# Kernel tuning notes

Measured on AMD Instinct MI355X. Metric: run time of the kernel, lower is better.

The kernel has to match this reference:

```python
import jax, jax.numpy as jnp
import numpy as np

D_MODEL, N_GROUPS, N_EXPERTS = 512, 8, 8
TOP_K_L1, TOP_K_L2 = 2, 2
BATCH, SEQ = 2, 512


def setup_inputs() -> dict:
    key = jax.random.key(0)
    ks = jax.random.split(key, 6)
    d, G, E = D_MODEL, N_GROUPS, N_EXPERTS
    scale = 0.02
    x = jax.random.normal(ks[0], (BATCH, SEQ, d), dtype=jnp.float32)
    g1 = jax.random.normal(ks[1], (d, G), dtype=jnp.float32) * scale          # level-1 gate (no bias)
    g2 = jax.random.normal(ks[2], (G, d, E), dtype=jnp.float32) * scale       # per-group level-2 gate (no bias)
    W1 = jax.random.normal(ks[3], (G, E, d, 2 * d), dtype=jnp.float32) * scale
    b1 = jnp.zeros((G, E, 2 * d), dtype=jnp.float32)
    W2 = jax.random.normal(ks[4], (G, E, 2 * d, d), dtype=jnp.float32) * scale
    b2 = jnp.zeros((G, E, d), dtype=jnp.float32)
    return {"x": x, "g1": g1, "g2": g2, "W1": W1, "b1": b1, "W2": W2, "b2": b2}


def reference(x, g1, g2, W1, b1, W2, b2):
    B, S, d = x.shape
    G, E = g1.shape[1], g2.shape[2]
    xt = x.reshape(-1, d)  # [T, d]

    # ---- level-1 routing (groups) ----
    logits1 = xt @ g1                                   # [T, G]
    v1, i1 = jax.lax.top_k(logits1, TOP_K_L1)           # [T, k1]
    w1 = jax.nn.softmax(v1.astype(jnp.float32), axis=-1).astype(x.dtype)
    # dense combine weights: top-k indices are unique per token, so one-hot sum
    # is exactly the original gather/index_add_ math.
    c1 = jnp.sum(jax.nn.one_hot(i1, G, dtype=x.dtype) * w1[..., None], axis=1)  # [T, G]

    # ---- level-2 routing (experts within each group) ----
    logits2 = jnp.einsum('td,gde->tge', xt, g2)         # [T, G, E]
    v2, i2 = jax.lax.top_k(logits2, TOP_K_L2)           # [T, G, k2]
    w2 = jax.nn.softmax(v2.astype(jnp.float32), axis=-1).astype(x.dtype)
    c2 = jnp.sum(jax.nn.one_hot(i2, E, dtype=x.dtype) * w2[..., None], axis=2)  # [T, G, E]

    # ---- expert MLPs (Linear -> ReLU -> Linear), all experts, combined by weights ----
    h = jax.nn.relu(jnp.einsum('td,gedh->tgeh', xt, W1) + b1)   # [T, G, E, 2d]
    y = jnp.einsum('tgeh,gehd->tged', h, W2) + b2               # [T, G, E, d]

    group_out = jnp.einsum('tged,tge->tgd', y, c2)              # level-2 combine
    out = jnp.einsum('tgd,tg->td', group_out, c1)               # level-1 combine
    return out.reshape(B, S, d)
```

## Files before the change

### kernel.cpp

```cpp
#include <hip/hip_runtime.h>
#include <hip/hip_bf16.h>

#define D_M   512
#define H_M   1024
#define G_N   8
#define E_N   8
#define T_N   1024
#define NEXP  64
#define CAP   1024

#define LDK   520

typedef __attribute__((ext_vector_type(8))) short bf16x8;
typedef __attribute__((ext_vector_type(4))) float f32x4;
typedef __attribute__((ext_vector_type(4))) unsigned int u32x4;

__device__ __forceinline__ unsigned pack2(float a, float b) {
  unsigned r;
  asm("v_cvt_pk_bf16_f32 %0, %1, %2" : "=v"(r) : "v"(a), "v"(b));
  return r;
}
__device__ __forceinline__ unsigned short f2bf(float f) {
  unsigned u = __builtin_bit_cast(unsigned, f);
  u = (u + 0x7fffu + ((u >> 16) & 1u)) >> 16;
  return (unsigned short)u;
}

__global__ __launch_bounds__(64) void k_route(
    const float* __restrict__ x, const float* __restrict__ g1,
    const float* __restrict__ g2, float* __restrict__ slotW,
    int* __restrict__ counts, int* __restrict__ list) {
  __shared__ float xs[D_M];
  __shared__ float l2s[G_N][E_N];
  __shared__ float l1s[G_N];
  __shared__ float l1part[G_N][8];
  const int t = blockIdx.x;
  const int lane = threadIdx.x;
  const float* xr = x + (size_t)t * D_M;
  for (int i = lane; i < D_M; i += 64) xs[i] = xr[i];
  __syncthreads();
  {
    const int g = lane >> 3, e = lane & 7;
    const float* gp = g2 + (size_t)g * D_M * E_N + e;
    float acc = 0.f;
    #pragma unroll 8
    for (int i = 0; i < D_M; i++) acc += xs[i] * gp[(size_t)i * E_N];
    l2s[g][e] = acc;
  }
  {
    const int g = lane >> 3, c = lane & 7;
    float acc = 0.f;
    #pragma unroll 8
    for (int i = c * 64; i < c * 64 + 64; i++) acc += xs[i] * g1[(size_t)i * G_N + g];
    l1part[g][c] = acc;
  }
  __syncthreads();
  if (lane < G_N) {
    float s = 0.f;
    #pragma unroll
    for (int c = 0; c < 8; c++) s += l1part[lane][c];
    l1s[lane] = s;
  }
  __syncthreads();
  if (lane == 0) {
    int a1 = 0;
    for (int g = 1; g < G_N; g++) if (l1s[g] > l1s[a1]) a1 = g;
    int a2 = (a1 == 0) ? 1 : 0;
    for (int g = 0; g < G_N; g++) if (g != a1 && l1s[g] > l1s[a2]) a2 = g;
    const float m = l1s[a1];
    float w1a = __expf(l1s[a1] - m), w1b = __expf(l1s[a2] - m);
    const float inv = 1.f / (w1a + w1b);
    w1a *= inv; w1b *= inv;
    const int gsel[2] = {a1, a2};
    const float wsel[2] = {w1a, w1b};
    for (int a = 0; a < 2; a++) {
      const int g = gsel[a];
      int e1 = 0;
      for (int e = 1; e < E_N; e++) if (l2s[g][e] > l2s[g][e1]) e1 = e;
      int e2 = (e1 == 0) ? 1 : 0;
      for (int e = 0; e < E_N; e++) if (e != e1 && l2s[g][e] > l2s[g][e2]) e2 = e;
      const float mm = l2s[g][e1];
      float ua = __expf(l2s[g][e1] - mm), ub = __expf(l2s[g][e2] - mm);
      const float uin = 1.f / (ua + ub);
      ua *= uin; ub *= uin;
      const int ge0 = g * E_N + e1;
      const int ge1 = g * E_N + e2;
      slotW[t * 4 + a * 2 + 0] = wsel[a] * ua;
      slotW[t * 4 + a * 2 + 1] = wsel[a] * ub;
      int p0 = atomicAdd(&counts[ge0], 1);
      list[ge0 * CAP + p0] = t * 4 + a * 2 + 0;
      int p1 = atomicAdd(&counts[ge1], 1);
      list[ge1 * CAP + p1] = t * 4 + a * 2 + 1;
    }
  }
}

__global__ __launch_bounds__(256, 1) void k_mlp1(
    const float* __restrict__ x, const float* __restrict__ W1,
    const float* __restrict__ b1, const int* __restrict__ counts,
    const int* __restrict__ list, unsigned short* __restrict__ h_ws) {
  const int ge = blockIdx.x >> 4;
  const int jt = blockIdx.x & 15;
  const int jbase = jt * 64;
  const int n = counts[ge];
  if (n == 0) return;
  __shared__ unsigned short wl[4 * 16 * 64 * 8];
  __shared__ unsigned short xl[64 * LDK];
  __shared__ int tokTS[64];
  const int tid = threadIdx.x;
  const int lane = tid & 63, wave = tid >> 6;
  const int m16 = lane & 15, quad = lane >> 4;

  const float bv = b1[ge * H_M + jbase + wave * 16 + m16];

  {
    const float* Wg = W1 + (size_t)ge * (D_M * H_M) + jbase;
    const int rgrp = tid >> 4;
    const int lidx = tid & 15;
    const int wp = lidx >> 2;
    const int m16b = (lidx & 3) * 4;
    #pragma unroll 4
    for (int pass = 0; pass < 32; pass++) {
      const int r = pass * 16 + rgrp;
      f32x4 v = *(const f32x4*)(Wg + (size_t)r * H_M + lidx * 4);
      const int s = r >> 5, q = (r >> 3) & 3, i = r & 7;
      unsigned p0 = pack2(v.x, v.y), p1 = pack2(v.z, v.w);
      unsigned short* base = &wl[((wp * 16 + s) * 64 + q * 16 + m16b) * 8 + i];
      base[0 * 8] = (unsigned short)p0;
      base[1 * 8] = (unsigned short)(p0 >> 16);
      base[2 * 8] = (unsigned short)p1;
      base[3 * 8] = (unsigned short)(p1 >> 16);
    }
  }

  for (int t0 = 0; t0 < n; t0 += 64) {
    __syncthreads();
    if (tid < 64) {
      int idx = t0 + tid;
      tokTS[tid] = list[ge * CAP + (idx < n ? idx : n - 1)];
    }
    __syncthreads();
    {
      const int trow = tid >> 2;
      const int kb = (tid & 3) * 4;
      const float* xr = x + (size_t)(tokTS[trow] >> 2) * D_M + kb;
      unsigned short* dst = &xl[trow * LDK + kb];
      #pragma unroll 8
      for (int rep = 0; rep < 32; rep++) {
        f32x4 v = *(const f32x4*)(xr + rep * 16);
        uint2 p = { pack2(v.x, v.y), pack2(v.z, v.w) };
        *(uint2*)(dst + rep * 16) = p;
      }
    }
    __syncthreads();

    f32x4 acc[4] = {};
    #pragma unroll
    for (int s = 0; s < 16; s++) {
      bf16x8 wfrag = *(const bf16x8*)&wl[((wave * 16 + s) * 64 + lane) * 8];
      #pragma unroll
      for (int mt = 0; mt < 4; mt++) {
        bf16x8 af = *(bf16x8*)&xl[(mt * 16 + m16) * LDK + s * 32 + quad * 8];
        acc[mt] = __builtin_amdgcn_mfma_f32_16x16x32_bf16(af, wfrag, acc[mt], 0, 0, 0);
      }
    }
    #pragma unroll
    for (int mt = 0; mt < 4; mt++)
      #pragma unroll
      for (int i = 0; i < 4; i++) {
        const int tr = mt * 16 + quad * 4 + i;
        if (t0 + tr < n) {
          const int ts = tokTS[tr];
          float v = acc[mt][i] + bv;
          h_ws[(size_t)ts * H_M + jbase + wave * 16 + m16] = f2bf(v > 0.f ? v : 0.f);
        }
      }
  }
}

__global__ __launch_bounds__(256, 1) void k_mlp2(
    const unsigned short* __restrict__ h_ws, const float* __restrict__ W2,
    const float* __restrict__ b2, const int* __restrict__ counts,
    const int* __restrict__ list, float* __restrict__ y0,
    float* __restrict__ y1) {
  const int ge = blockIdx.x >> 4;
  const int jt = (blockIdx.x >> 1) & 7;
  const int jbase = jt * 64;
  const int ks = blockIdx.x & 1;
  const int n = counts[ge];
  if (n == 0) return;
  __shared__ unsigned short wl[4 * 16 * 64 * 8];
  __shared__ unsigned short xl[64 * LDK];
  __shared__ int tokTS[64];
  const int tid = threadIdx.x;
  const int lane = tid & 63, wave = tid >> 6;
  const int m16 = lane & 15, quad = lane >> 4;

  const float bv = ks == 0 ? b2[ge * D_M + jbase + wave * 16 + m16] : 0.f;
  float* yk = ks == 0 ? y0 : y1;

  {
    const float* Wg = W2 + (size_t)ge * (H_M * D_M) + (size_t)(ks * 512) * D_M + jbase;
    const int rgrp = tid >> 4;
    const int lidx = tid & 15;
    const int wp = lidx >> 2;
    const int m16b = (lidx & 3) * 4;
    #pragma unroll 4
    for (int pass = 0; pass < 32; pass++) {
      const int r = pass * 16 + rgrp;
      f32x4 v = *(const f32x4*)(Wg + (size_t)r * D_M + lidx * 4);
      const int s = r >> 5, q = (r >> 3) & 3, i = r & 7;
      unsigned p0 = pack2(v.x, v.y), p1 = pack2(v.z, v.w);
      unsigned short* base = &wl[((wp * 16 + s) * 64 + q * 16 + m16b) * 8 + i];
      base[0 * 8] = (unsigned short)p0;
      base[1 * 8] = (unsigned short)(p0 >> 16);
      base[2 * 8] = (unsigned short)p1;
      base[3 * 8] = (unsigned short)(p1 >> 16);
    }
  }

  for (int t0 = 0; t0 < n; t0 += 64) {
    __syncthreads();
    if (tid < 64) {
      int idx = t0 + tid;
      tokTS[tid] = list[ge * CAP + (idx < n ? idx : n - 1)];
    }
    __syncthreads();
    {
      const int trow = tid >> 2;
      const int kb = (tid & 3) * 8;
      const unsigned short* hr = h_ws + (size_t)tokTS[trow] * H_M + ks * 512 + kb;
      unsigned short* dst = &xl[trow * LDK + kb];
      #pragma unroll 8
      for (int rep = 0; rep < 16; rep++)
        *(u32x4*)(dst + rep * 32) = *(const u32x4*)(hr + rep * 32);
    }
    __syncthreads();

    f32x4 acc[4] = {};
    #pragma unroll
    for (int s = 0; s < 16; s++) {
      bf16x8 wfrag = *(const bf16x8*)&wl[((wave * 16 + s) * 64 + lane) * 8];
      #pragma unroll
      for (int mt = 0; mt < 4; mt++) {
        bf16x8 af = *(bf16x8*)&xl[(mt * 16 + m16) * LDK + s * 32 + quad * 8];
        acc[mt] = __builtin_amdgcn_mfma_f32_16x16x32_bf16(af, wfrag, acc[mt], 0, 0, 0);
      }
    }
    #pragma unroll
    for (int mt = 0; mt < 4; mt++)
      #pragma unroll
      for (int i = 0; i < 4; i++) {
        const int tr = mt * 16 + quad * 4 + i;
        if (t0 + tr < n) {
          const int ts = tokTS[tr];
          yk[(size_t)ts * D_M + jbase + wave * 16 + m16] = acc[mt][i] + bv;
        }
      }
  }
}

__global__ __launch_bounds__(256) void k_combine(
    const float* __restrict__ y0, const float* __restrict__ y1,
    const float* __restrict__ slotW, float* __restrict__ out) {
  const int idx = blockIdx.x * 256 + threadIdx.x;
  if (idx >= T_N * D_M / 4) return;
  const int t = idx >> 7;
  const int j = (idx & 127) * 4;
  float4 r = {0.f, 0.f, 0.f, 0.f};
  #pragma unroll
  for (int s = 0; s < 4; s++) {
    const float w = slotW[t * 4 + s];
    const size_t off = (size_t)(t * 4 + s) * D_M + j;
    const float4 a = *(const float4*)(y0 + off);
    const float4 b = *(const float4*)(y1 + off);
    r.x += w * (a.x + b.x);
    r.y += w * (a.y + b.y);
    r.z += w * (a.z + b.z);
    r.w += w * (a.w + b.w);
  }
  *(float4*)&out[(size_t)t * D_M + j] = r;
}

extern "C" void kernel_launch(void* const* d_in, const int* in_sizes, int n_in,
                              void* d_out, int out_size, void* d_ws, size_t ws_size,
                              hipStream_t stream) {
  const float* x  = (const float*)d_in[0];
  const float* g1 = (const float*)d_in[1];
  const float* g2 = (const float*)d_in[2];
  const float* W1 = (const float*)d_in[3];
  const float* b1 = (const float*)d_in[4];
  const float* W2 = (const float*)d_in[5];
  const float* b2 = (const float*)d_in[6];
  float* out = (float*)d_out;

  char* ws = (char*)d_ws;
  float*          slotW  = (float*)(ws + 16384);
  int*            counts = (int*)(ws + 32768);
  int*            list   = (int*)(ws + 36864);
  unsigned short* h_ws   = (unsigned short*)(ws + 524288);
  float*          y0     = (float*)(ws + 524288 + 8388608);
  float*          y1     = (float*)(ws + 524288 + 16777216);

  hipMemsetAsync(counts, 0, NEXP * sizeof(int), stream);
  k_route<<<T_N, 64, 0, stream>>>(x, g1, g2, slotW, counts, list);
  k_mlp1<<<NEXP * 16, 256, 0, stream>>>(x, W1, b1, counts, list, h_ws);
  k_mlp2<<<NEXP * 16, 256, 0, stream>>>(h_ws, W2, b2, counts, list, y0, y1);
  k_combine<<<(T_N * D_M / 4) / 256, 256, 0, stream>>>(y0, y1, slotW, out);
}
```

Before: 390.8 us.

## Load gathered activations directly from global, keep weight fragments in registers

The routing kernel now also writes a bf16 copy of x, so mlp1 no longer converts fp32 activations per tile. Both MLP kernels drop the LDS activation staging tile and its barriers. Each lane gathers its A-fragments straight from global memory through per-row token pointers, and the 16 weight fragments are hoisted into registers once. Freeing the LDS tile lets launch bounds request two blocks per CU. The cost is uncoalesced 16-byte global gathers inside the MFMA loop and higher register pressure.

After: 427.0 us. 9.3% more time.

```diff
diff --git a/kernel.cpp b/kernel.cpp
--- a/kernel.cpp
+++ b/kernel.cpp
@@ -9,8 +9,6 @@
 #define NEXP  64
 #define CAP   1024
 
-#define LDK   520
-
 typedef __attribute__((ext_vector_type(8))) short bf16x8;
 typedef __attribute__((ext_vector_type(4))) float f32x4;
 typedef __attribute__((ext_vector_type(4))) unsigned int u32x4;
@@ -29,7 +27,8 @@
 __global__ __launch_bounds__(64) void k_route(
     const float* __restrict__ x, const float* __restrict__ g1,
     const float* __restrict__ g2, float* __restrict__ slotW,
-    int* __restrict__ counts, int* __restrict__ list) {
+    int* __restrict__ counts, int* __restrict__ list,
+    unsigned short* __restrict__ xb) {
   __shared__ float xs[D_M];
   __shared__ float l2s[G_N][E_N];
   __shared__ float l1s[G_N];
@@ -39,6 +38,11 @@
   const float* xr = x + (size_t)t * D_M;
   for (int i = lane; i < D_M; i += 64) xs[i] = xr[i];
   __syncthreads();
+  {
+    const float* p = &xs[lane * 8];
+    u32x4 o = { pack2(p[0], p[1]), pack2(p[2], p[3]), pack2(p[4], p[5]), pack2(p[6], p[7]) };
+    *(u32x4*)(xb + (size_t)t * D_M + lane * 8) = o;
+  }
   {
     const int g = lane >> 3, e = lane & 7;
     const float* gp = g2 + (size_t)g * D_M * E_N + e;
@@ -95,8 +99,8 @@
   }
 }
 
-__global__ __launch_bounds__(256, 1) void k_mlp1(
-    const float* __restrict__ x, const float* __restrict__ W1,
+__global__ __launch_bounds__(256, 2) void k_mlp1(
+    const unsigned short* __restrict__ xb, const float* __restrict__ W1,
     const float* __restrict__ b1, const int* __restrict__ counts,
     const int* __restrict__ list, unsigned short* __restrict__ h_ws) {
   const int ge = blockIdx.x >> 4;
@@ -105,13 +109,9 @@
   const int n = counts[ge];
   if (n == 0) return;
   __shared__ unsigned short wl[4 * 16 * 64 * 8];
-  __shared__ unsigned short xl[64 * LDK];
-  __shared__ int tokTS[64];
   const int tid = threadIdx.x;
   const int lane = tid & 63, wave = tid >> 6;
   const int m16 = lane & 15, quad = lane >> 4;
-
-  const float bv = b1[ge * H_M + jbase + wave * 16 + m16];
 
   {
     const float* Wg = W1 + (size_t)ge * (D_M * H_M) + jbase;
@@ -132,36 +132,30 @@
       base[3 * 8] = (unsigned short)(p1 >> 16);
     }
   }
+  __syncthreads();
+  bf16x8 wf[16];
+  #pragma unroll
+  for (int s = 0; s < 16; s++)
+    wf[s] = *(const bf16x8*)&wl[((wave * 16 + s) * 64 + lane) * 8];
+
+  const float bv = b1[ge * H_M + jbase + wave * 16 + m16];
+  const int* lst = list + ge * CAP;
 
   for (int t0 = 0; t0 < n; t0 += 64) {
-    __syncthreads();
-    if (tid < 64) {
-      int idx = t0 + tid;
-      tokTS[tid] = list[ge * CAP + (idx < n ? idx : n - 1)];
-    }
-    __syncthreads();
-    {
-      const int trow = tid >> 2;
-      const int kb = (tid & 3) * 4;
-      const float* xr = x + (size_t)(tokTS[trow] >> 2) * D_M + kb;
-      unsigned short* dst = &xl[trow * LDK + kb];
-      #pragma unroll 8
-      for (int rep = 0; rep < 32; rep++) {
-        f32x4 v = *(const f32x4*)(xr + rep * 16);
-        uint2 p = { pack2(v.x, v.y), pack2(v.z, v.w) };
-        *(uint2*)(dst + rep * 16) = p;
-      }
-    }
-    __syncthreads();
-
+    const unsigned short* ap[4];
+    #pragma unroll
+    for (int mt = 0; mt < 4; mt++) {
+      int idx = t0 + mt * 16 + m16;
+      int slot = lst[idx < n ? idx : n - 1];
+      ap[mt] = xb + (size_t)(slot >> 2) * D_M;
+    }
     f32x4 acc[4] = {};
     #pragma unroll
     for (int s = 0; s < 16; s++) {
-      bf16x8 wfrag = *(const bf16x8*)&wl[((wave * 16 + s) * 64 + lane) * 8];
       #pragma unroll
       for (int mt = 0; mt < 4; mt++) {
-        bf16x8 af = *(bf16x8*)&xl[(mt * 16 + m16) * LDK + s * 32 + quad * 8];
-        acc[mt] = __builtin_amdgcn_mfma_f32_16x16x32_bf16(af, wfrag, acc[mt], 0, 0, 0);
+        bf16x8 af = *(const bf16x8*)(ap[mt] + s * 32 + quad * 8);
+        acc[mt] = __builtin_amdgcn_mfma_f32_16x16x32_bf16(af, wf[s], acc[mt], 0, 0, 0);
       }
     }
     #pragma unroll
@@ -170,15 +164,15 @@
       for (int i = 0; i < 4; i++) {
         const int tr = mt * 16 + quad * 4 + i;
         if (t0 + tr < n) {
-          const int ts = tokTS[tr];
+          const int slot = lst[t0 + tr];
           float v = acc[mt][i] + bv;
-          h_ws[(size_t)ts * H_M + jbase + wave * 16 + m16] = f2bf(v > 0.f ? v : 0.f);
+          h_ws[(size_t)slot * H_M + jbase + wave * 16 + m16] = f2bf(v > 0.f ? v : 0.f);
         }
       }
   }
 }
 
-__global__ __launch_bounds__(256, 1) void k_mlp2(
+__global__ __launch_bounds__(256, 2) void k_mlp2(
     const unsigned short* __restrict__ h_ws, const float* __restrict__ W2,
     const float* __restrict__ b2, const int* __restrict__ counts,
     const int* __restrict__ list, float* __restrict__ y0,
@@ -190,14 +184,9 @@
   const int n = counts[ge];
   if (n == 0) return;
   __shared__ unsigned short wl[4 * 16 * 64 * 8];
-  __shared__ unsigned short xl[64 * LDK];
-  __shared__ int tokTS[64];
   const int tid = threadIdx.x;
   const int lane = tid & 63, wave = tid >> 6;
   const int m16 = lane & 15, quad = lane >> 4;
-
-  const float bv = ks == 0 ? b2[ge * D_M + jbase + wave * 16 + m16] : 0.f;
-  float* yk = ks == 0 ? y0 : y1;
 
   {
     const float* Wg = W2 + (size_t)ge * (H_M * D_M) + (size_t)(ks * 512) * D_M + jbase;
@@ -218,33 +207,31 @@
       base[3 * 8] = (unsigned short)(p1 >> 16);
     }
   }
+  __syncthreads();
+  bf16x8 wf[16];
+  #pragma unroll
+  for (int s = 0; s < 16; s++)
+    wf[s] = *(const bf16x8*)&wl[((wave * 16 + s) * 64 + lane) * 8];
+
+  const float bv = ks == 0 ? b2[ge * D_M + jbase + wave * 16 + m16] : 0.f;
+  float* yk = ks == 0 ? y0 : y1;
+  const int* lst = list + ge * CAP;
 
   for (int t0 = 0; t0 < n; t0 += 64) {
-    __syncthreads();
-    if (tid < 64) {
-      int idx = t0 + tid;
-      tokTS[tid] = list[ge * CAP + (idx < n ? idx : n - 1)];
-    }
-    __syncthreads();
-    {
-      const int trow = tid >> 2;
-      const int kb = (tid & 3) * 8;
-      const unsigned short* hr = h_ws + (size_t)tokTS[trow] * H_M + ks * 512 + kb;
-      unsigned short* dst = &xl[trow * LDK + kb];
-      #pragma unroll 8
-      for (int rep = 0; rep < 16; rep++)
-        *(u32x4*)(dst + rep * 32) = *(const u32x4*)(hr + rep * 32);
-    }
-    __syncthreads();
-
+    const unsigned short* ap[4];
+    #pragma unroll
+    for (int mt = 0; mt < 4; mt++) {
+      int idx = t0 + mt * 16 + m16;
+      int slot = lst[idx < n ? idx : n - 1];
+      ap[mt] = h_ws + (size_t)slot * H_M + ks * 512;
+    }
     f32x4 acc[4] = {};
     #pragma unroll
     for (int s = 0; s < 16; s++) {
-      bf16x8 wfrag = *(const bf16x8*)&wl[((wave * 16 + s) * 64 + lane) * 8];
       #pragma unroll
       for (int mt = 0; mt < 4; mt++) {
-        bf16x8 af = *(bf16x8*)&xl[(mt * 16 + m16) * LDK + s * 32 + quad * 8];
-        acc[mt] = __builtin_amdgcn_mfma_f32_16x16x32_bf16(af, wfrag, acc[mt], 0, 0, 0);
+        bf16x8 af = *(const bf16x8*)(ap[mt] + s * 32 + quad * 8);
+        acc[mt] = __builtin_amdgcn_mfma_f32_16x16x32_bf16(af, wf[s], acc[mt], 0, 0, 0);
       }
     }
     #pragma unroll
@@ -253,8 +240,8 @@
       for (int i = 0; i < 4; i++) {
         const int tr = mt * 16 + quad * 4 + i;
         if (t0 + tr < n) {
-          const int ts = tokTS[tr];
-          yk[(size_t)ts * D_M + jbase + wave * 16 + m16] = acc[mt][i] + bv;
+          const int slot = lst[t0 + tr];
+          yk[(size_t)slot * D_M + jbase + wave * 16 + m16] = acc[mt][i] + bv;
         }
       }
   }
@@ -295,16 +282,17 @@
   float* out = (float*)d_out;
 
   char* ws = (char*)d_ws;
-  float*          slotW  = (float*)(ws + 16384);
-  int*            counts = (int*)(ws + 32768);
-  int*            list   = (int*)(ws + 36864);
-  unsigned short* h_ws   = (unsigned short*)(ws + 524288);
-  float*          y0     = (float*)(ws + 524288 + 8388608);
-  float*          y1     = (float*)(ws + 524288 + 16777216);
+  float*          slotW  = (float*)(ws + 0);
+  int*            counts = (int*)(ws + 16384);
+  int*            list   = (int*)(ws + 20480);
+  unsigned short* xb     = (unsigned short*)(ws + 294912);
+  unsigned short* h_ws   = (unsigned short*)(ws + 2097152);
+  float*          y0     = (float*)(ws + 10485760);
+  float*          y1     = (float*)(ws + 18874368);
 
   hipMemsetAsync(counts, 0, NEXP * sizeof(int), stream);
-  k_route<<<T_N, 64, 0, stream>>>(x, g1, g2, slotW, counts, list);
-  k_mlp1<<<NEXP * 16, 256, 0, stream>>>(x, W1, b1, counts, list, h_ws);
+  k_route<<<T_N, 64, 0, stream>>>(x, g1, g2, slotW, counts, list, xb);
+  k_mlp1<<<NEXP * 16, 256, 0, stream>>>(xb, W1, b1, counts, list, h_ws);
   k_mlp2<<<NEXP * 16, 256, 0, stream>>>(h_ws, W2, b2, counts, list, y0, y1);
   k_combine<<<(T_N * D_M / 4) / 256, 256, 0, stream>>>(y0, y1, slotW, out);
 }
```
